# Kernel optimization log

Hardware: AMD Instinct MI355X
Metric: run time of the kernel (lower is better)

Reference implementation:

```python
import jax, jax.numpy as jnp
import numpy as np

NUM_EMBEDDINGS = 2048
EMBEDDING_DIM = 512
COMMITMENT_COST = 0.25


def setup_inputs() -> dict:
    key = jax.random.key(0)
    k1, k2 = jax.random.split(key)
    IP_score = jax.random.normal(k1, (256, 51, 512), dtype=jnp.float32)
    emb_weight = jax.random.normal(k2, (NUM_EMBEDDINGS, EMBEDDING_DIM), dtype=jnp.float32)
    return {"IP_score": IP_score, "emb_weight": emb_weight}


def reference(IP_score, emb_weight):
    sg = jax.lax.stop_gradient
    bs, kpts, seq = IP_score.shape
    x = IP_score.reshape(bs, kpts // 3, 3, seq)          # [bs, kpts/3, 3, D]
    flat = x.reshape(-1, seq)                             # [N, D], N = bs*kpts

    # pairwise squared L2 distances to codebook: [N, K]
    d = (jnp.sum(flat * flat, axis=1, keepdims=True)
         + jnp.sum(emb_weight * emb_weight, axis=1)
         - 2.0 * flat @ emb_weight.T)

    # nearest (argmin) and the 3rd-smallest index (coding_idx[:, 2] in torch)
    _, idx3 = jax.lax.top_k(-d, 3)                        # ascending distance order
    nearest = idx3[:, 0]
    third = idx3[:, 2]

    quantized = jnp.take(emb_weight, nearest, axis=0).reshape(x.shape)
    second_quantized = jnp.take(emb_weight, third, axis=0).reshape(x.shape)

    # commitment loss (quantized is detached in the original)
    e_latent_loss = jnp.mean((sg(quantized) - x) ** 2)
    k_loss = COMMITMENT_COST * e_latent_loss

    # straight-through estimator
    quantized_st = x + sg(quantized - x)
    second_st = x + sg(second_quantized - x)

    feature_EMA = quantized_st.reshape(bs, kpts, seq)
    sec_EMA = second_st.reshape(bs, kpts, seq)

    cp_score = 1.0 - (jnp.linalg.norm(feature_EMA - IP_score)
                      / jnp.linalg.norm(sec_EMA - IP_score))
    return (cp_score, k_loss, feature_EMA)
```

## Files before the change

kernel.cpp:

```cpp
#include <hip/hip_runtime.h>
#include <hip/hip_bf16.h>
#include <math.h>

#define RM 13056
#define KD 512
#define NE 2048
#define NELEM 6684672.0

#define BM 128
#define BN 128
#define BK 32
#define NKT (KD / BK)
#define NBLK (NE / BN)
#define NCAND (NBLK * 4)
#define NTAIL (RM / 4)

typedef __attribute__((ext_vector_type(8))) short bf16x8;
typedef __attribute__((ext_vector_type(4))) float f32x4;
typedef unsigned long long ull;

__device__ __forceinline__ void dma16(const void* g, void* l) {
  __builtin_amdgcn_global_load_lds((const __attribute__((address_space(1))) void*)g,
                                   (__attribute__((address_space(3))) void*)l, 16, 0, 0);
}

__device__ __forceinline__ ull packdi(float d, int ix) {
  unsigned u = __float_as_uint(d);
  u ^= (unsigned)((int)u >> 31) | 0x80000000u;
  return ((ull)u << 32) | (unsigned)ix;
}

#define XB (RM * 64 / 256)
#define EB (NE * 64 / 256)
#define NB (NE / 4)
__device__ __forceinline__ void split_chunks(const float* __restrict__ src,
                                             unsigned short* __restrict__ hi,
                                             int rows, int o) {
  int t4 = o >> 2;
  int kt = t4 / rows;
  int row = t4 - kt * rows;
  int slot = o & 3;
  int q = slot ^ ((row >> 1) & 3);
  const float* s = src + (size_t)row * KD + kt * 32 + q * 8;
  float4 v0 = ((const float4*)s)[0];
  float4 v1 = ((const float4*)s)[1];
  float f[8] = {v0.x, v0.y, v0.z, v0.w, v1.x, v1.y, v1.z, v1.w};
  unsigned hh[4];
#pragma unroll
  for (int j = 0; j < 4; ++j) {
    __hip_bfloat16 b0 = __float2bfloat16(f[2 * j]);
    __hip_bfloat16 b1 = __float2bfloat16(f[2 * j + 1]);
    hh[j] = (unsigned)*(unsigned short*)&b0 | ((unsigned)*(unsigned short*)&b1 << 16);
  }
  ((uint4*)hi)[o] = make_uint4(hh[0], hh[1], hh[2], hh[3]);
}

__global__ __launch_bounds__(256) void k_prep(const float* __restrict__ X,
                                              const float* __restrict__ E,
                                              unsigned short* __restrict__ Xh,
                                              unsigned short* __restrict__ Eh,
                                              float* __restrict__ EN) {
  const int b = blockIdx.x, tid = threadIdx.x;
  if (b < XB) {
    split_chunks(X, Xh, RM, b * 256 + tid);
  } else if (b < XB + EB) {
    split_chunks(E, Eh, NE, (b - XB) * 256 + tid);
  } else {
    int n = (b - XB - EB) * 4 + (tid >> 6);
    int lane = tid & 63;
    const float* e = E + (size_t)n * KD;
    float s = 0.f;
#pragma unroll
    for (int j = 0; j < 8; ++j) { float v = e[lane + 64 * j]; s += v * v; }
#pragma unroll
    for (int off = 32; off; off >>= 1) s += __shfl_down(s, off);
    if (lane == 0) EN[n] = s;
  }
}

__device__ __forceinline__ int chidx(int row, int q) {
  return (row * 4 + (q ^ ((row >> 1) & 3))) * 8;
}

__global__ __launch_bounds__(256, 4) void k_dist_bf16(
    const unsigned short* __restrict__ Xh,
    const unsigned short* __restrict__ Eh,
    const float* __restrict__ EN, ull* __restrict__ cand) {
  __shared__ __align__(16) unsigned short sXh[2][BM * BK];
  __shared__ __align__(16) unsigned short sEh[2][BN * BK];
  __shared__ float sEN[BN];

  const int tid = threadIdx.x;
  const int lane = tid & 63;
  const int w = tid >> 6;
  const int quad = lane >> 4;
  const int lx = lane & 15;
  const int by = blockIdx.x & (NBLK - 1);
  const int bx = blockIdx.x >> 4;
  const int rowBase = bx * BM;
  const int colBase = by * BN;

  if (tid < BN) sEN[tid] = EN[colBase + tid];

  int aidx[2], bidx[8];
#pragma unroll
  for (int mt = 0; mt < 2; ++mt) aidx[mt] = chidx(w * 32 + mt * 16 + lx, quad);
#pragma unroll
  for (int ct = 0; ct < 8; ++ct) bidx[ct] = chidx(ct * 16 + lx, quad);

  f32x4 acc[2][8];
#pragma unroll
  for (int mt = 0; mt < 2; ++mt)
#pragma unroll
    for (int ct = 0; ct < 8; ++ct) acc[mt][ct] = (f32x4){0.f, 0.f, 0.f, 0.f};

  auto stage = [&](int h, int kt) {
    const size_t xbase = ((size_t)kt * RM + rowBase) * 4;
    const size_t ebase = ((size_t)kt * NE + colBase) * 4;
#pragma unroll
    for (int i = 0; i < 2; ++i) {
      const int c = i * 256 + tid;
      const int ldsOff = (i * 256 + w * 64) * 8;
      dma16(Xh + (xbase + c) * 8, &sXh[h][ldsOff]);
      dma16(Eh + (ebase + c) * 8, &sEh[h][ldsOff]);
    }
  };

  auto compute = [&](int h) {
    bf16x8 Ah[2];
#pragma unroll
    for (int mt = 0; mt < 2; ++mt) Ah[mt] = *(const bf16x8*)&sXh[h][aidx[mt]];
#pragma unroll
    for (int ct = 0; ct < 8; ++ct) {
      bf16x8 Bh = *(const bf16x8*)&sEh[h][bidx[ct]];
#pragma unroll
      for (int mt = 0; mt < 2; ++mt)
        acc[mt][ct] = __builtin_amdgcn_mfma_f32_16x16x32_bf16(Ah[mt], Bh, acc[mt][ct], 0, 0, 0);
    }
  };

#pragma unroll 1
  for (int kt2 = 0; kt2 < NKT / 2; ++kt2) {
    __syncthreads();
    stage(0, kt2 * 2);
    stage(1, kt2 * 2 + 1);
    __syncthreads();
    compute(0);
    compute(1);
  }

  float en[8];
#pragma unroll
  for (int ct = 0; ct < 8; ++ct) en[ct] = sEN[ct * 16 + lx];

#pragma unroll
  for (int mt = 0; mt < 2; ++mt) {
#pragma unroll
    for (int j = 0; j < 4; ++j) {
      float a0 = 3.4e38f, a1 = 3.4e38f, a2 = 3.4e38f, a3 = 3.4e38f;
      int i0 = 0x7fffffff, i1 = i0, i2 = i0, i3 = i0;
#pragma unroll
      for (int ct = 0; ct < 8; ++ct) {
        float d = en[ct] - 2.0f * acc[mt][ct][j];
        int ix = colBase + ct * 16 + lx;
        if (d < a3) {
          if (d < a2) { a3 = a2; i3 = i2;
            if (d < a1) { a2 = a1; i2 = i1;
              if (d < a0) { a1 = a0; i1 = i0; a0 = d; i0 = ix; }
              else { a1 = d; i1 = ix; } }
            else { a2 = d; i2 = ix; } }
          else { a3 = d; i3 = ix; }
        }
      }
      ull k0 = packdi(a0, i0), k1 = packdi(a1, i1);
      ull k2 = packdi(a2, i2), k3 = packdi(a3, i3);
      int pos = 0;
      ull res[4];
#pragma unroll
      for (int r = 0; r < 4; ++r) {
        ull h = pos == 0 ? k0 : pos == 1 ? k1 : pos == 2 ? k2 : pos == 3 ? k3 : ~0ull;
        ull m = h;
#pragma unroll
        for (int step = 1; step < 16; step <<= 1) {
          ull o = __shfl_xor(m, step, 16);
          m = o < m ? o : m;
        }
        res[r] = m;
        pos += (h == m) ? 1 : 0;
      }
      if (lx == 0) {
        int row = rowBase + w * 32 + mt * 16 + quad * 4 + j;
        ull* dst = cand + (size_t)row * NCAND + by * 4;
        dst[0] = res[0]; dst[1] = res[1]; dst[2] = res[2]; dst[3] = res[3];
      }
    }
  }
}

__device__ __forceinline__ void refine_core(const float* __restrict__ X,
                                            const float* __restrict__ E,
                                            const int* ci, int row,
                                            float* __restrict__ outF,
                                            double* __restrict__ part) {
  const int w = threadIdx.x >> 6, lane = threadIdx.x & 63;
  __shared__ double bs1[4], bs3[4];
  const float* xr = X + (size_t)row * KD;
  float4 x0 = *(const float4*)(xr + lane * 8);
  float4 x1 = *(const float4*)(xr + lane * 8 + 4);
  double a[8];
#pragma unroll
  for (int c = 0; c < 8; ++c) {
    const float* er = E + (size_t)ci[c] * KD;
    float4 e0 = *(const float4*)(er + lane * 8);
    float4 e1 = *(const float4*)(er + lane * 8 + 4);
    double s = 0.0;
    double d0 = (double)e0.x - (double)x0.x; s += d0 * d0;
    double d1 = (double)e0.y - (double)x0.y; s += d1 * d1;
    double d2 = (double)e0.z - (double)x0.z; s += d2 * d2;
    double d3 = (double)e0.w - (double)x0.w; s += d3 * d3;
    double d4 = (double)e1.x - (double)x1.x; s += d4 * d4;
    double d5 = (double)e1.y - (double)x1.y; s += d5 * d5;
    double d6 = (double)e1.z - (double)x1.z; s += d6 * d6;
    double d7 = (double)e1.w - (double)x1.w; s += d7 * d7;
    a[c] = s;
  }
#pragma unroll
  for (int c = 0; c < 8; ++c)
#pragma unroll
    for (int off = 32; off; off >>= 1) a[c] += __shfl_down(a[c], off);
  int best = 0;
  if (lane == 0) {
    double d[8]; int id[8];
#pragma unroll
    for (int c = 0; c < 8; ++c) { d[c] = a[c]; id[c] = ci[c]; }
    for (int i = 0; i < 8; ++i)
      for (int j = i + 1; j < 8; ++j)
        if (d[j] < d[i] || (d[j] == d[i] && id[j] < id[i])) {
          double dt = d[i]; d[i] = d[j]; d[j] = dt;
          int it = id[i]; id[i] = id[j]; id[j] = it;
        }
    bs1[w] = d[0];
    bs3[w] = d[2];
    best = id[0];
  }
  best = __shfl(best, 0);
  const float* er = E + (size_t)best * KD;
  *(float4*)(outF + (size_t)row * KD + lane * 8) = *(const float4*)(er + lane * 8);
  *(float4*)(outF + (size_t)row * KD + lane * 8 + 4) = *(const float4*)(er + lane * 8 + 4);
  __syncthreads();
  if (threadIdx.x == 0) {
    part[blockIdx.x * 2] = bs1[0] + bs1[1] + bs1[2] + bs1[3];
    part[blockIdx.x * 2 + 1] = bs3[0] + bs3[1] + bs3[2] + bs3[3];
  }
}

__device__ __forceinline__ ull sort64(ull k, int lane) {
#pragma unroll
  for (int kk = 2; kk <= 64; kk <<= 1) {
#pragma unroll
    for (int j = kk >> 1; j > 0; j >>= 1) {
      ull o = __shfl_xor(k, j, 64);
      bool dirUp = (lane & kk) == 0;
      bool lower = (lane & j) == 0;
      bool pl = o < k;
      bool take = (dirUp == lower) ? pl : !pl;
      if (take) k = o;
    }
  }
  return k;
}

__global__ __launch_bounds__(256) void k_mrf(const float* __restrict__ X,
                                             const float* __restrict__ E,
                                             const ull* __restrict__ cand,
                                             float* __restrict__ outF,
                                             double* __restrict__ part) {
  const int lane = threadIdx.x & 63;
  const int row = blockIdx.x * 4 + (threadIdx.x >> 6);
  ull k = lane < NCAND ? cand[(size_t)row * NCAND + lane] : ~0ull;
  k = sort64(k, lane);
  int ci[8];
#pragma unroll
  for (int c = 0; c < 8; ++c) ci[c] = (int)(__shfl(k, c, 64) & 0xffffffffull);
  refine_core(X, E, ci, row, outF, part);
}

__global__ __launch_bounds__(256) void k_fin(const double* __restrict__ part,
                                             float* __restrict__ out) {
  const int tid = threadIdx.x;
  double a1 = 0.0, a3 = 0.0;
  for (int r = tid; r < NTAIL; r += 256) { a1 += part[2 * r]; a3 += part[2 * r + 1]; }
#pragma unroll
  for (int off = 32; off; off >>= 1) {
    a1 += __shfl_down(a1, off);
    a3 += __shfl_down(a3, off);
  }
  __shared__ double s1[4], s3[4];
  const int w = tid >> 6, lane = tid & 63;
  if (lane == 0) { s1[w] = a1; s3[w] = a3; }
  __syncthreads();
  if (tid == 0) {
    double S1 = s1[0] + s1[1] + s1[2] + s1[3];
    double S3 = s3[0] + s3[1] + s3[2] + s3[3];
    out[0] = (float)(1.0 - sqrt(S1 / S3));
    out[1] = (float)(0.25 * S1 / NELEM);
  }
}

__global__ __launch_bounds__(256) void k_merge(const ull* __restrict__ cand,
                                               int* __restrict__ top8) {
  const int lane = threadIdx.x & 63;
  const int row = blockIdx.x * 4 + (threadIdx.x >> 6);
  ull k = lane < NCAND ? cand[(size_t)row * NCAND + lane] : ~0ull;
  k = sort64(k, lane);
  if (lane < 8) top8[(size_t)row * 8 + lane] = (int)(k & 0xffffffffull);
}

__global__ __launch_bounds__(256) void k_refine_fb(const float* __restrict__ X,
                                                   const float* __restrict__ E,
                                                   const int* __restrict__ top8,
                                                   float* __restrict__ outF,
                                                   double* __restrict__ part) {
  const int row = blockIdx.x * 4 + (threadIdx.x >> 6);
  int ci[8];
#pragma unroll
  for (int c = 0; c < 8; ++c) ci[c] = top8[(size_t)row * 8 + c];
  refine_core(X, E, ci, row, outF, part);
}

extern "C" void kernel_launch(void* const* d_in, const int* in_sizes, int n_in,
                              void* d_out, int out_size, void* d_ws, size_t ws_size,
                              hipStream_t stream) {
  const float* IP = (const float*)d_in[0];
  const float* EMB = (const float*)d_in[1];
  float* out = (float*)d_out;

  char* ws = (char*)d_ws;
  size_t off = 0;
  float* EN = (float*)(ws + off);        off += NE * 4;
  double* part = (double*)(ws + off);    off += (size_t)NTAIL * 2 * 8;
  int* top8 = (int*)(ws + off);          off += (size_t)RM * 8 * 4;
  unsigned short* Xh = (unsigned short*)(ws + off); off += (size_t)RM * KD * 2;
  unsigned short* Ehs = (unsigned short*)(ws + off); off += (size_t)NE * KD * 2;
  ull* candWs = (ull*)(ws + off);        off += (size_t)RM * NCAND * 8;
  const bool fused = ws_size >= off;

  ull* cand = fused ? candWs : (ull*)(out + 2);

  hipLaunchKernelGGL(k_prep, dim3(XB + EB + NB), dim3(256), 0, stream,
                     IP, EMB, Xh, Ehs, EN);
  hipLaunchKernelGGL(k_dist_bf16, dim3((RM / BM) * NBLK), dim3(256), 0, stream,
                     Xh, Ehs, EN, cand);
  if (fused) {
    hipLaunchKernelGGL(k_mrf, dim3(NTAIL), dim3(256), 0, stream,
                       IP, EMB, cand, out + 2, part);
  } else {
    hipLaunchKernelGGL(k_merge, dim3(NTAIL), dim3(256), 0, stream, cand, top8);
    hipLaunchKernelGGL(k_refine_fb, dim3(NTAIL), dim3(256), 0, stream,
                       IP, EMB, top8, out + 2, part);
  }
  hipLaunchKernelGGL(k_fin, dim3(1), dim3(256), 0, stream, part, out);
}
```

Before: 175.3 us.

## Fold final reduction into refine kernel via last-block atomic counter

Removes the separate single-block k_fin launch in the fused path. Each k_mrf block bumps a global atomic counter after writing its partial sums, and the last block to finish performs the final double-precision reduction and writes both scalar outputs; the counter is reset in k_prep. The distance GEMM staging also switches from recomputing global addresses every step to incrementing precomputed byte pointers. The aim is to save one kernel launch plus a little address arithmetic, at the cost of an atomic and a thread fence per block.

```diff
diff --git a/kernel.cpp b/kernel.cpp
--- a/kernel.cpp
+++ b/kernel.cpp
@@ -59,8 +59,10 @@
                                               const float* __restrict__ E,
                                               unsigned short* __restrict__ Xh,
                                               unsigned short* __restrict__ Eh,
-                                              float* __restrict__ EN) {
+                                              float* __restrict__ EN,
+                                              unsigned* __restrict__ cnt) {
   const int b = blockIdx.x, tid = threadIdx.x;
+  if (b == 0 && tid == 0) cnt[0] = 0;
   if (b < XB) {
     split_chunks(X, Xh, RM, b * 256 + tid);
   } else if (b < XB + EB) {
@@ -114,15 +116,17 @@
 #pragma unroll
     for (int ct = 0; ct < 8; ++ct) acc[mt][ct] = (f32x4){0.f, 0.f, 0.f, 0.f};
 
-  auto stage = [&](int h, int kt) {
-    const size_t xbase = ((size_t)kt * RM + rowBase) * 4;
-    const size_t ebase = ((size_t)kt * NE + colBase) * 4;
+  const char* gX = (const char*)Xh + (size_t)(rowBase * 4 + tid) * 16;
+  const char* gE = (const char*)Eh + (size_t)(colBase * 4 + tid) * 16;
+  constexpr size_t strideX = (size_t)RM * 64;
+  constexpr size_t strideE = (size_t)NE * 64;
+
+  auto stage = [&](int h) {
 #pragma unroll
     for (int i = 0; i < 2; ++i) {
-      const int c = i * 256 + tid;
       const int ldsOff = (i * 256 + w * 64) * 8;
-      dma16(Xh + (xbase + c) * 8, &sXh[h][ldsOff]);
-      dma16(Eh + (ebase + c) * 8, &sEh[h][ldsOff]);
+      dma16(gX + i * 4096, &sXh[h][ldsOff]);
+      dma16(gE + i * 4096, &sEh[h][ldsOff]);
     }
   };
 
@@ -142,8 +146,8 @@
 #pragma unroll 1
   for (int kt2 = 0; kt2 < NKT / 2; ++kt2) {
     __syncthreads();
-    stage(0, kt2 * 2);
-    stage(1, kt2 * 2 + 1);
+    stage(0); gX += strideX; gE += strideE;
+    stage(1); gX += strideX; gE += strideE;
     __syncthreads();
     compute(0);
     compute(1);
@@ -274,15 +278,46 @@
                                              const float* __restrict__ E,
                                              const ull* __restrict__ cand,
                                              float* __restrict__ outF,
-                                             double* __restrict__ part) {
-  const int lane = threadIdx.x & 63;
-  const int row = blockIdx.x * 4 + (threadIdx.x >> 6);
+                                             double* __restrict__ part,
+                                             unsigned* __restrict__ cnt,
+                                             float* __restrict__ out) {
+  const int tid = threadIdx.x;
+  const int lane = tid & 63;
+  const int row = blockIdx.x * 4 + (tid >> 6);
   ull k = lane < NCAND ? cand[(size_t)row * NCAND + lane] : ~0ull;
   k = sort64(k, lane);
   int ci[8];
 #pragma unroll
   for (int c = 0; c < 8; ++c) ci[c] = (int)(__shfl(k, c, 64) & 0xffffffffull);
   refine_core(X, E, ci, row, outF, part);
+
+  __shared__ int sLast;
+  if (tid == 0) {
+    __threadfence();
+    unsigned t = atomicAdd(cnt, 1u);
+    sLast = (t == NTAIL - 1);
+  }
+  __syncthreads();
+  if (sLast) {
+    __threadfence();
+    double a1 = 0.0, a3 = 0.0;
+    for (int r = tid; r < NTAIL; r += 256) { a1 += part[2 * r]; a3 += part[2 * r + 1]; }
+#pragma unroll
+    for (int off = 32; off; off >>= 1) {
+      a1 += __shfl_down(a1, off);
+      a3 += __shfl_down(a3, off);
+    }
+    __shared__ double s1[4], s3[4];
+    const int w = tid >> 6;
+    if (lane == 0) { s1[w] = a1; s3[w] = a3; }
+    __syncthreads();
+    if (tid == 0) {
+      double S1 = s1[0] + s1[1] + s1[2] + s1[3];
+      double S3 = s3[0] + s3[1] + s3[2] + s3[3];
+      out[0] = (float)(1.0 - sqrt(S1 / S3));
+      out[1] = (float)(0.25 * S1 / NELEM);
+    }
+  }
 }
 
 __global__ __launch_bounds__(256) void k_fin(const double* __restrict__ part,
@@ -339,6 +374,7 @@
   size_t off = 0;
   float* EN = (float*)(ws + off);        off += NE * 4;
   double* part = (double*)(ws + off);    off += (size_t)NTAIL * 2 * 8;
+  unsigned* cnt = (unsigned*)(ws + off); off += 16;
   int* top8 = (int*)(ws + off);          off += (size_t)RM * 8 * 4;
   unsigned short* Xh = (unsigned short*)(ws + off); off += (size_t)RM * KD * 2;
   unsigned short* Ehs = (unsigned short*)(ws + off); off += (size_t)NE * KD * 2;
@@ -348,16 +384,16 @@
   ull* cand = fused ? candWs : (ull*)(out + 2);
 
   hipLaunchKernelGGL(k_prep, dim3(XB + EB + NB), dim3(256), 0, stream,
-                     IP, EMB, Xh, Ehs, EN);
+                     IP, EMB, Xh, Ehs, EN, cnt);
   hipLaunchKernelGGL(k_dist_bf16, dim3((RM / BM) * NBLK), dim3(256), 0, stream,
                      Xh, Ehs, EN, cand);
   if (fused) {
     hipLaunchKernelGGL(k_mrf, dim3(NTAIL), dim3(256), 0, stream,
-                       IP, EMB, cand, out + 2, part);
+                       IP, EMB, cand, out + 2, part, cnt, out);
   } else {
     hipLaunchKernelGGL(k_merge, dim3(NTAIL), dim3(256), 0, stream, cand, top8);
     hipLaunchKernelGGL(k_refine_fb, dim3(NTAIL), dim3(256), 0, stream,
                        IP, EMB, top8, out + 2, part);
-  }
-  hipLaunchKernelGGL(k_fin, dim3(1), dim3(256), 0, stream, part, out);
-}
+    hipLaunchKernelGGL(k_fin, dim3(1), dim3(256), 0, stream, part, out);
+  }
+}
```

Result: slower. 295.6 us (+68.6%).
